# Kernel optimization log

Hardware: AMD Instinct MI355X
Metric: run time of the kernel (lower is better)

Reference implementation:

```python
import jax, jax.numpy as jnp
import numpy as np

N_NODES = 40000
N_EDGES = 640000
IN_C = 128
HID = 32
HEADS = 4
OUT_C = 8
NUM_GRAPHS = 64
NEG_SLOPE = 0.2


def setup_inputs() -> dict:
    key = jax.random.key(0)
    ks = jax.random.split(key, 16)
    x = jax.random.normal(ks[0], (N_NODES, IN_C), dtype=jnp.float32)
    edge_index = jax.random.randint(ks[1], (2, N_EDGES), 0, N_NODES, dtype=jnp.int64)
    batch = jnp.sort(jax.random.randint(ks[2], (N_NODES,), 0, NUM_GRAPHS, dtype=jnp.int64))
    s = lambda k, shape, fan_in: jax.random.normal(k, shape, jnp.float32) / np.sqrt(fan_in)
    # conv0: in -> hid, 4 heads, concat
    W0 = s(ks[3], (IN_C, HEADS * HID), IN_C)
    a_src0 = s(ks[4], (HEADS, HID), HID)
    a_dst0 = s(ks[5], (HEADS, HID), HID)
    b0 = jnp.zeros((HEADS * HID,), jnp.float32)
    # conv1: hid*H -> hid, 4 heads, concat
    W1 = s(ks[6], (HEADS * HID, HEADS * HID), HEADS * HID)
    a_src1 = s(ks[7], (HEADS, HID), HID)
    a_dst1 = s(ks[8], (HEADS, HID), HID)
    b1 = jnp.zeros((HEADS * HID,), jnp.float32)
    # conv2: hid*H -> hid, 1 head, no concat
    W2 = s(ks[9], (HEADS * HID, HID), HEADS * HID)
    a_src2 = s(ks[10], (1, HID), HID)
    a_dst2 = s(ks[11], (1, HID), HID)
    b2 = jnp.zeros((HID,), jnp.float32)
    lin1_w = s(ks[12], (HID, IN_C), HID)
    lin1_b = jnp.zeros((IN_C,), jnp.float32)
    lin2_w = s(ks[13], (IN_C, OUT_C), IN_C)
    lin2_b = jnp.zeros((OUT_C,), jnp.float32)
    return dict(x=x, edge_index=edge_index, batch=batch,
                W0=W0, a_src0=a_src0, a_dst0=a_dst0, b0=b0,
                W1=W1, a_src1=a_src1, a_dst1=a_dst1, b1=b1,
                W2=W2, a_src2=a_src2, a_dst2=a_dst2, b2=b2,
                lin1_w=lin1_w, lin1_b=lin1_b, lin2_w=lin2_w, lin2_b=lin2_b)


def gat_conv(x, src, dst, W, a_src, a_dst, b, heads, out_c, concat):
    N = x.shape[0]
    h = (x @ W).reshape(N, heads, out_c)          # [N,H,C]
    als = (h * a_src[None]).sum(-1)               # [N,H]
    ald = (h * a_dst[None]).sum(-1)               # [N,H]
    e = jax.nn.leaky_relu(als[src] + ald[dst], NEG_SLOPE)  # [E,H]
    m = jax.ops.segment_max(e, dst, num_segments=N)
    m = jnp.where(jnp.isfinite(m), m, 0.0)
    p = jnp.exp(e - m[dst])                       # [E,H]
    denom = jax.ops.segment_sum(p, dst, num_segments=N)
    alpha = p / jnp.maximum(denom[dst], 1e-16)
    out = jax.ops.segment_sum(h[src] * alpha[:, :, None], dst, num_segments=N)
    out = out.reshape(N, heads * out_c) if concat else out.mean(axis=1)
    return out + b


def reference(x, edge_index, batch,
              W0, a_src0, a_dst0, b0,
              W1, a_src1, a_dst1, b1,
              W2, a_src2, a_dst2, b2,
              lin1_w, lin1_b, lin2_w, lin2_b):
    N = x.shape[0]
    # PyG GATConv adds self-loops by default
    loop = jnp.arange(N, dtype=edge_index.dtype)
    src = jnp.concatenate([edge_index[0], loop])
    dst = jnp.concatenate([edge_index[1], loop])
    # eval mode: dropout is identity
    h = jax.nn.elu(gat_conv(x, src, dst, W0, a_src0, a_dst0, b0, HEADS, HID, True))
    h = jax.nn.elu(gat_conv(h, src, dst, W1, a_src1, a_dst1, b1, HEADS, HID, True))
    h = jax.nn.elu(gat_conv(h, src, dst, W2, a_src2, a_dst2, b2, 1, HID, False))
    # global mean pool over graphs
    sums = jax.ops.segment_sum(h, batch, num_segments=NUM_GRAPHS)
    cnts = jax.ops.segment_sum(jnp.ones((N, 1), h.dtype), batch, num_segments=NUM_GRAPHS)
    g = sums / jnp.maximum(cnts, 1.0)             # [G, HID]
    g = jax.nn.relu(g @ lin1_w + lin1_b)
    return g @ lin2_w + lin2_b                    # [G, OUT_C]
```

## Files before the change

kernel.cpp:

```cpp
#include <hip/hip_runtime.h>
#include <hip/hip_bf16.h>

#define N_NODES 40000
#define N_EDGES 640000
#define E_TOT   (N_EDGES + N_NODES)
#define NUM_GRAPHS 64
#define SCAN_BLOCKS 160
#define SCAN_CHUNK  250

#define CVTX_BLOCKS 5000
#define CVTW_BLOCKS 144
#define ZERO_INTS   (N_NODES + NUM_GRAPHS * 32 + NUM_GRAPHS)
#define ZERO_BLOCKS ((ZERO_INTS + 255) / 256)

typedef __attribute__((ext_vector_type(8))) short bf16x8;
typedef __attribute__((ext_vector_type(4))) float f32x4;

__device__ inline float bf2f(unsigned short u) {
    union { unsigned int i; float f; } v; v.i = ((unsigned int)u) << 16; return v.f;
}
__device__ inline unsigned short f2bf(float f) {
    union { float f; unsigned int i; } v; v.f = f;
    unsigned int r = v.i + 0x7FFF + ((v.i >> 16) & 1);
    return (unsigned short)(r >> 16);
}


__global__ __launch_bounds__(256) void setup_kernel(const float* __restrict__ x,
                                                    const float* __restrict__ W0,
                                                    const float* __restrict__ W1,
                                                    const float* __restrict__ W2,
                                                    unsigned short* __restrict__ Xb,
                                                    unsigned short* __restrict__ Wt0,
                                                    unsigned short* __restrict__ Wt1,
                                                    unsigned short* __restrict__ Wt2,
                                                    int* __restrict__ zbase) {
    int b = blockIdx.x;
    int tid = threadIdx.x;
    if (b < CVTX_BLOCKS) {
        int i = b * 256 + tid;
        float4 v = ((const float4*)x)[i];
        ushort4 o;
        o.x = f2bf(v.x); o.y = f2bf(v.y); o.z = f2bf(v.z); o.w = f2bf(v.w);
        ((ushort4*)Xb)[i] = o;
    } else if (b < CVTX_BLOCKS + CVTW_BLOCKS) {
        int idx = (b - CVTX_BLOCKS) * 256 + tid;
        if (idx < 16384) {
            int n = idx >> 7, k = idx & 127;
            Wt0[idx] = f2bf(W0[k * 128 + n]);
        } else if (idx < 32768) {
            int i = idx - 16384;
            int n = i >> 7, k = i & 127;
            Wt1[i] = f2bf(W1[k * 128 + n]);
        } else {
            int i = idx - 32768;
            int n = i >> 7, k = i & 127;
            Wt2[i] = f2bf(W2[k * 32 + n]);
        }
    } else {
        int i = (b - CVTX_BLOCKS - CVTW_BLOCKS) * 256 + tid;
        if (i < ZERO_INTS) zbase[i] = 0;
    }
}


__global__ __launch_bounds__(256) void hist_rank_kernel(const int* __restrict__ edst,
                                                        int* __restrict__ counts,
                                                        int* __restrict__ rank) {
    int e = blockIdx.x * 256 + threadIdx.x;
    if (e >= E_TOT) return;
    int d = (e < N_EDGES) ? edst[e] : (e - N_EDGES);
    rank[e] = atomicAdd(&counts[d], 1);
}

__global__ __launch_bounds__(256) void bsum_kernel(const int* __restrict__ counts,
                                                   int* __restrict__ bsum) {
    __shared__ int ws[4];
    int b = blockIdx.x, tid = threadIdx.x;
    int idx = b * SCAN_CHUNK + tid;
    int v = (tid < SCAN_CHUNK) ? counts[idx] : 0;
#pragma unroll
    for (int off = 32; off >= 1; off >>= 1) v += __shfl_down(v, off, 64);
    if ((tid & 63) == 0) ws[tid >> 6] = v;
    __syncthreads();
    if (tid == 0) bsum[b] = ws[0] + ws[1] + ws[2] + ws[3];
}

__global__ __launch_bounds__(256) void bscan_kernel(const int* __restrict__ bsum,
                                                    int* __restrict__ bofs) {
    __shared__ int s[256];
    int tid = threadIdx.x;
    int v = (tid < SCAN_BLOCKS) ? bsum[tid] : 0;
    s[tid] = v;
    __syncthreads();
    for (int off = 1; off < 256; off <<= 1) {
        int t = (tid >= off) ? s[tid - off] : 0;
        __syncthreads();
        s[tid] += t;
        __syncthreads();
    }
    if (tid < SCAN_BLOCKS) bofs[tid] = s[tid] - v;
}

__global__ __launch_bounds__(256) void boffs_kernel(const int* __restrict__ counts,
                                                    const int* __restrict__ bofs,
                                                    int* __restrict__ offs) {
    __shared__ int s[256];
    int b = blockIdx.x, tid = threadIdx.x;
    int idx = b * SCAN_CHUNK + tid;
    int v = (tid < SCAN_CHUNK) ? counts[idx] : 0;
    s[tid] = v;
    __syncthreads();
    for (int off = 1; off < 256; off <<= 1) {
        int t = (tid >= off) ? s[tid - off] : 0;
        __syncthreads();
        s[tid] += t;
        __syncthreads();
    }
    int incl = s[tid];
    int base = bofs[b];
    if (tid < SCAN_CHUNK) {
        offs[idx] = base + incl - v;
        if (idx == N_NODES - 1) offs[N_NODES] = base + incl;
    }
}

__global__ __launch_bounds__(256) void scatter_kernel(const int* __restrict__ esrc,
                                                      const int* __restrict__ edst,
                                                      const int* __restrict__ offs,
                                                      const int* __restrict__ rank,
                                                      int* __restrict__ ssrc) {
    int e = blockIdx.x * 256 + threadIdx.x;
    if (e >= E_TOT) return;
    int d, s;
    if (e < N_EDGES) { d = edst[e]; s = esrc[e]; }
    else             { d = e - N_EDGES; s = d; }
    ssrc[offs[d] + rank[e]] = s;
}

__global__ __launch_bounds__(256) void gemm128_mfma(const unsigned short* __restrict__ Xb,
                                                    const unsigned short* __restrict__ Wt,
                                                    const float* __restrict__ asrc,
                                                    const float* __restrict__ adst,
                                                    unsigned short* __restrict__ Hb,
                                                    float* __restrict__ ALS_t,
                                                    float* __restrict__ ALD_t) {
    int wave = threadIdx.x >> 6;
    int lane = threadIdx.x & 63;
    int l15 = lane & 15;
    int q = lane >> 4;
    int r0 = (blockIdx.x * 4 + wave) * 16;

    f32x4 acc[8];
#pragma unroll
    for (int t = 0; t < 8; ++t) acc[t] = (f32x4){0.f, 0.f, 0.f, 0.f};

    float asv[8], adv[8];
#pragma unroll
    for (int t = 0; t < 8; ++t) {
        int c = t * 16 + l15;
        asv[t] = asrc[c];
        adv[t] = adst[c];
    }

    const unsigned short* xrow = Xb + (long)(r0 + l15) * 128 + q * 8;
    const unsigned short* wrow = Wt + (long)l15 * 128 + q * 8;
#pragma unroll
    for (int kt = 0; kt < 4; ++kt) {
        bf16x8 a = *(const bf16x8*)(xrow + kt * 32);
#pragma unroll
        for (int t = 0; t < 8; ++t) {
            bf16x8 b = *(const bf16x8*)(wrow + (long)t * 16 * 128 + kt * 32);
            acc[t] = __builtin_amdgcn_mfma_f32_16x16x32_bf16(a, b, acc[t], 0, 0, 0);
        }
    }

#pragma unroll
    for (int t = 0; t < 8; ++t)
#pragma unroll
        for (int i = 0; i < 4; ++i)
            Hb[(long)(r0 + q * 4 + i) * 128 + t * 16 + l15] = f2bf(acc[t][i]);

#pragma unroll
    for (int i = 0; i < 4; ++i) {
        float ps0 = acc[0][i] * asv[0] + acc[1][i] * asv[1];
        float ps1 = acc[2][i] * asv[2] + acc[3][i] * asv[3];
        float ps2 = acc[4][i] * asv[4] + acc[5][i] * asv[5];
        float ps3 = acc[6][i] * asv[6] + acc[7][i] * asv[7];
        float pd0 = acc[0][i] * adv[0] + acc[1][i] * adv[1];
        float pd1 = acc[2][i] * adv[2] + acc[3][i] * adv[3];
        float pd2 = acc[4][i] * adv[4] + acc[5][i] * adv[5];
        float pd3 = acc[6][i] * adv[6] + acc[7][i] * adv[7];
#pragma unroll
        for (int m = 1; m < 16; m <<= 1) {
            ps0 += __shfl_xor(ps0, m, 16); ps1 += __shfl_xor(ps1, m, 16);
            ps2 += __shfl_xor(ps2, m, 16); ps3 += __shfl_xor(ps3, m, 16);
            pd0 += __shfl_xor(pd0, m, 16); pd1 += __shfl_xor(pd1, m, 16);
            pd2 += __shfl_xor(pd2, m, 16); pd3 += __shfl_xor(pd3, m, 16);
        }
        int r = r0 + q * 4 + i;
        if (l15 < 4) {
            float v = (l15 == 0) ? ps0 : (l15 == 1) ? ps1 : (l15 == 2) ? ps2 : ps3;
            ALS_t[l15 * N_NODES + r] = v;
        } else if (l15 < 8) {
            int h = l15 - 4;
            float v = (h == 0) ? pd0 : (h == 1) ? pd1 : (h == 2) ? pd2 : pd3;
            ALD_t[h * N_NODES + r] = v;
        }
    }
}

__global__ __launch_bounds__(256) void gemm32_mfma(const unsigned short* __restrict__ Xb,
                                                   const unsigned short* __restrict__ Wt2,
                                                   const float* __restrict__ asrc,
                                                   const float* __restrict__ adst,
                                                   unsigned short* __restrict__ H2b,
                                                   float* __restrict__ ALS,
                                                   float* __restrict__ ALD) {
    int wave = threadIdx.x >> 6;
    int lane = threadIdx.x & 63;
    int l15 = lane & 15;
    int q = lane >> 4;
    int r0 = (blockIdx.x * 4 + wave) * 16;

    f32x4 acc[2];
    acc[0] = (f32x4){0.f, 0.f, 0.f, 0.f};
    acc[1] = (f32x4){0.f, 0.f, 0.f, 0.f};

    const unsigned short* xrow = Xb + (long)(r0 + l15) * 128 + q * 8;
    const unsigned short* wrow = Wt2 + (long)l15 * 128 + q * 8;
#pragma unroll
    for (int kt = 0; kt < 4; ++kt) {
        bf16x8 a = *(const bf16x8*)(xrow + kt * 32);
#pragma unroll
        for (int t = 0; t < 2; ++t) {
            bf16x8 b = *(const bf16x8*)(wrow + (long)t * 16 * 128 + kt * 32);
            acc[t] = __builtin_amdgcn_mfma_f32_16x16x32_bf16(a, b, acc[t], 0, 0, 0);
        }
    }

    float as0 = asrc[l15], as1 = asrc[16 + l15];
    float ad0 = adst[l15], ad1 = adst[16 + l15];
#pragma unroll
    for (int t = 0; t < 2; ++t)
#pragma unroll
        for (int i = 0; i < 4; ++i)
            H2b[(long)(r0 + q * 4 + i) * 32 + t * 16 + l15] = f2bf(acc[t][i]);

#pragma unroll
    for (int i = 0; i < 4; ++i) {
        float ps = acc[0][i] * as0 + acc[1][i] * as1;
        float pd = acc[0][i] * ad0 + acc[1][i] * ad1;
#pragma unroll
        for (int m = 1; m < 16; m <<= 1) {
            ps += __shfl_xor(ps, m, 16);
            pd += __shfl_xor(pd, m, 16);
        }
        if (l15 == 0) {
            int r = r0 + q * 4 + i;
            ALS[r] = ps;
            ALD[r] = pd;
        }
    }
}

__global__ __launch_bounds__(256) void agg128(const unsigned short* __restrict__ Hb,
                                              const float* __restrict__ ALS_t,
                                              const float* __restrict__ ALD_t,
                                              const int* __restrict__ offs,
                                              const int* __restrict__ ssrc,
                                              const float* __restrict__ bias,
                                              unsigned short* __restrict__ OUTb) {
    int n = blockIdx.x * 4 + (threadIdx.x >> 6);
    n = __builtin_amdgcn_readfirstlane(n);
    if (n >= N_NODES) return;
    int lane = threadIdx.x & 63;
    int c = lane * 2;
    int head = lane >> 4;
    int e16 = lane & 15;
    float aldh = ALD_t[head * N_NODES + n];
    const float* alsh = ALS_t + (long)head * N_NODES;
    int j0 = __builtin_amdgcn_readfirstlane(offs[n]);
    int j1 = __builtin_amdgcn_readfirstlane(offs[n + 1]);
    float a0 = 0.f, a1 = 0.f, dsum = 0.f;
    for (int jb = j0; jb < j1; jb += 16) {
        int j = jb + e16;
        int jc = (j < j1) ? j : (j1 - 1);
        int s = ssrc[jc];
        float e = alsh[s] + aldh;
        e = (e > 0.f) ? e : 0.2f * e;
        float w = (j < j1) ? __expf(e) : 0.f;
        int st[16]; float wt[16];
#pragma unroll
        for (int t = 0; t < 16; ++t) {
            st[t] = __shfl(s, t, 16);
            wt[t] = __shfl(w, t, 16);
        }
        unsigned int hv[16];
#pragma unroll
        for (int t = 0; t < 16; ++t)
            hv[t] = *(const unsigned int*)(Hb + (long)st[t] * 128 + c);
#pragma unroll
        for (int t = 0; t < 16; ++t) {
            float h0 = bf2f((unsigned short)(hv[t] & 0xFFFF));
            float h1 = bf2f((unsigned short)(hv[t] >> 16));
            dsum += wt[t];
            a0 += wt[t] * h0;
            a1 += wt[t] * h1;
        }
    }
    float inv = 1.0f / dsum;
    float o0 = a0 * inv + bias[c];
    float o1 = a1 * inv + bias[c + 1];
    o0 = (o0 > 0.f) ? o0 : (__expf(o0) - 1.f);
    o1 = (o1 > 0.f) ? o1 : (__expf(o1) - 1.f);
    ushort2 ob; ob.x = f2bf(o0); ob.y = f2bf(o1);
    *(ushort2*)(OUTb + (long)n * 128 + c) = ob;
}

__global__ __launch_bounds__(256) void agg32(const unsigned short* __restrict__ H2b,
                                             const float* __restrict__ ALS,
                                             const float* __restrict__ ALD,
                                             const int* __restrict__ offs,
                                             const int* __restrict__ ssrc,
                                             const float* __restrict__ bias,
                                             float* __restrict__ OUT) {
    int wv = blockIdx.x * 4 + (threadIdx.x >> 6);
    int lane = threadIdx.x & 63;
    int col = lane & 31;
    int half = lane >> 5;
    int e16 = lane & 15;
    int n = wv * 2 + half;
    if (n >= N_NODES) return;
    float aldn = ALD[n];
    int j0 = offs[n], j1 = offs[n + 1];
    float a = 0.f, dsum = 0.f;
    for (int jb = j0; jb < j1; jb += 16) {
        int j = jb + e16;
        int jc = (j < j1) ? j : (j1 - 1);
        int s = ssrc[jc];
        float e = ALS[s] + aldn;
        e = (e > 0.f) ? e : 0.2f * e;
        float w = (j < j1) ? __expf(e) : 0.f;
        int st[16]; float wt[16];
#pragma unroll
        for (int t = 0; t < 16; ++t) {
            st[t] = __shfl(s, t, 16);
            wt[t] = __shfl(w, t, 16);
        }
        unsigned short hv[16];
#pragma unroll
        for (int t = 0; t < 16; ++t)
            hv[t] = H2b[st[t] * 32 + col];
#pragma unroll
        for (int t = 0; t < 16; ++t) {
            dsum += wt[t];
            a += wt[t] * bf2f(hv[t]);
        }
    }
    float o = a / dsum + bias[col];
    o = (o > 0.f) ? o : (__expf(o) - 1.f);
    OUT[n * 32 + col] = o;
}

__global__ __launch_bounds__(256) void pool_kernel(const float* __restrict__ H3,
                                                   const int* __restrict__ batch,
                                                   float* __restrict__ gsum,
                                                   float* __restrict__ gcnt) {
    const int CHUNK = 40;
    int gid = (blockIdx.x * 256 + threadIdx.x) >> 5;
    int c = threadIdx.x & 31;
    int n0 = gid * CHUNK;
    if (n0 >= N_NODES) return;
    int n1 = n0 + CHUNK;
    if (n1 > N_NODES) n1 = N_NODES;
    int cur = batch[n0];
    float acc = 0.f;
    int cnt = 0;
    for (int n = n0; n < n1; ++n) {
        int b = batch[n];
        if (b != cur) {
            atomicAdd(&gsum[cur * 32 + c], acc);
            if (c == 0) atomicAdd(&gcnt[cur], (float)cnt);
            cur = b; acc = 0.f; cnt = 0;
        }
        acc += H3[n * 32 + c];
        cnt++;
    }
    atomicAdd(&gsum[cur * 32 + c], acc);
    if (c == 0) atomicAdd(&gcnt[cur], (float)cnt);
}

__global__ __launch_bounds__(256) void mlp_kernel(const float* __restrict__ gsum,
                                                  const float* __restrict__ gcnt,
                                                  const float* __restrict__ l1w,
                                                  const float* __restrict__ l1b,
                                                  const float* __restrict__ l2w,
                                                  const float* __restrict__ l2b,
                                                  float* __restrict__ out) {
    __shared__ float g[NUM_GRAPHS * 32];
    __shared__ float t1[NUM_GRAPHS * 128];
    int tid = threadIdx.x;
    for (int i = tid; i < NUM_GRAPHS * 32; i += 256) {
        float c = gcnt[i >> 5];
        g[i] = gsum[i] / fmaxf(c, 1.0f);
    }
    __syncthreads();
    for (int i = tid; i < NUM_GRAPHS * 128; i += 256) {
        int r = i >> 7, j = i & 127;
        float a = l1b[j];
        for (int k = 0; k < 32; ++k) a += g[r * 32 + k] * l1w[k * 128 + j];
        t1[i] = fmaxf(a, 0.f);
    }
    __syncthreads();
    for (int i = tid; i < NUM_GRAPHS * 8; i += 256) {
        int r = i >> 3, j = i & 7;
        float a = l2b[j];
        for (int k = 0; k < 128; ++k) a += t1[r * 128 + k] * l2w[k * 8 + j];
        out[i] = a;
    }
}


extern "C" void kernel_launch(void* const* d_in, const int* in_sizes, int n_in,
                              void* d_out, int out_size, void* d_ws, size_t ws_size,
                              hipStream_t stream) {
    const float* x      = (const float*)d_in[0];
    const int*   eidx   = (const int*)d_in[1];
    const int*   batch  = (const int*)d_in[2];
    const float* W0     = (const float*)d_in[3];
    const float* asrc0  = (const float*)d_in[4];
    const float* adst0  = (const float*)d_in[5];
    const float* b0     = (const float*)d_in[6];
    const float* W1     = (const float*)d_in[7];
    const float* asrc1  = (const float*)d_in[8];
    const float* adst1  = (const float*)d_in[9];
    const float* b1     = (const float*)d_in[10];
    const float* W2     = (const float*)d_in[11];
    const float* asrc2  = (const float*)d_in[12];
    const float* adst2  = (const float*)d_in[13];
    const float* b2     = (const float*)d_in[14];
    const float* l1w    = (const float*)d_in[15];
    const float* l1b    = (const float*)d_in[16];
    const float* l2w    = (const float*)d_in[17];
    const float* l2b    = (const float*)d_in[18];
    float* out = (float*)d_out;

    const int* esrc = eidx;
    const int* edst = eidx + N_EDGES;

    float* ALS  = (float*)d_ws;
    float* ALD  = ALS + N_NODES * 4;
    float* h3   = ALD + N_NODES * 4;
    int* counts = (int*)(h3 + (long)N_NODES * 32);
    float* gsum = (float*)(counts + N_NODES);
    float* gcnt = gsum + NUM_GRAPHS * 32;
    int* offs   = (int*)(gcnt + NUM_GRAPHS);
    int* bsum   = offs + (N_NODES + 1);
    int* bofs   = bsum + SCAN_BLOCKS;
    int* rank   = bofs + SCAN_BLOCKS;
    int* ssrc   = rank + E_TOT;
    uintptr_t p = (uintptr_t)(ssrc + E_TOT);
    p = (p + 15) & ~(uintptr_t)15;
    unsigned short* Xb   = (unsigned short*)p;
    unsigned short* Hb   = Xb + (long)N_NODES * 128;
    unsigned short* OUTb = Hb + (long)N_NODES * 128;
    unsigned short* H2b  = OUTb + (long)N_NODES * 128;
    unsigned short* Wt0  = H2b + (long)N_NODES * 32;
    unsigned short* Wt1  = Wt0 + 128 * 128;
    unsigned short* Wt2  = Wt1 + 128 * 128;

    setup_kernel<<<CVTX_BLOCKS + CVTW_BLOCKS + ZERO_BLOCKS, 256, 0, stream>>>(
        x, W0, W1, W2, Xb, Wt0, Wt1, Wt2, counts);

    int eblocks = (E_TOT + 255) / 256;
    hist_rank_kernel<<<eblocks, 256, 0, stream>>>(edst, counts, rank);
    bsum_kernel<<<SCAN_BLOCKS, 256, 0, stream>>>(counts, bsum);
    bscan_kernel<<<1, 256, 0, stream>>>(bsum, bofs);
    boffs_kernel<<<SCAN_BLOCKS, 256, 0, stream>>>(counts, bofs, offs);
    scatter_kernel<<<eblocks, 256, 0, stream>>>(esrc, edst, offs, rank, ssrc);

    gemm128_mfma<<<625, 256, 0, stream>>>(Xb, Wt0, asrc0, adst0, Hb, ALS, ALD);
    agg128<<<10000, 256, 0, stream>>>(Hb, ALS, ALD, offs, ssrc, b0, OUTb);

    gemm128_mfma<<<625, 256, 0, stream>>>(OUTb, Wt1, asrc1, adst1, Hb, ALS, ALD);
    agg128<<<10000, 256, 0, stream>>>(Hb, ALS, ALD, offs, ssrc, b1, OUTb);

    gemm32_mfma<<<625, 256, 0, stream>>>(OUTb, Wt2, asrc2, adst2, H2b, ALS, ALD);
    agg32<<<5000, 256, 0, stream>>>(H2b, ALS, ALD, offs, ssrc, b2, h3);

    pool_kernel<<<125, 256, 0, stream>>>(h3, batch, gsum, gcnt);
    mlp_kernel<<<1, 256, 0, stream>>>(gsum, gcnt, l1w, l1b, l2w, l2b, out);
}
```

Baseline: 313.5 us.

## Split hidden features into per-head planes and aggregate one head per wave

The GEMM now writes its output as four head-major planes of 32 bf16 columns per node instead of one 128-wide row. The 128-wide aggregation launches four times as many blocks, one per (head, block of nodes). Each wave handles one head, with its four 16-lane groups gathering different neighbours, and the partial sums are reduced across groups with shuffles. The intent is smaller per-head working sets for better cache locality and more parallelism for the gather. The cost is redundant index and offset loads per head, extra shuffles, and only 16 of 64 lanes doing the final store.

```diff
diff --git a/kernel.cpp b/kernel.cpp
--- a/kernel.cpp
+++ b/kernel.cpp
@@ -142,7 +142,7 @@
                                                     const unsigned short* __restrict__ Wt,
                                                     const float* __restrict__ asrc,
                                                     const float* __restrict__ adst,
-                                                    unsigned short* __restrict__ Hb,
+                                                    unsigned short* __restrict__ Hq,
                                                     float* __restrict__ ALS_t,
                                                     float* __restrict__ ALD_t) {
     int wave = threadIdx.x >> 6;
@@ -176,10 +176,12 @@
     }
 
 #pragma unroll
-    for (int t = 0; t < 8; ++t)
+    for (int t = 0; t < 8; ++t) {
+        unsigned short* hq = Hq + (long)(t >> 1) * N_NODES * 32;
 #pragma unroll
         for (int i = 0; i < 4; ++i)
-            Hb[(long)(r0 + q * 4 + i) * 128 + t * 16 + l15] = f2bf(acc[t][i]);
+            hq[(long)(r0 + q * 4 + i) * 32 + (t & 1) * 16 + l15] = f2bf(acc[t][i]);
+    }
 
 #pragma unroll
     for (int i = 0; i < 4; ++i) {
@@ -264,22 +266,22 @@
     }
 }
 
-__global__ __launch_bounds__(256) void agg128(const unsigned short* __restrict__ Hb,
+__global__ __launch_bounds__(256) void agg128(const unsigned short* __restrict__ Hq,
                                               const float* __restrict__ ALS_t,
                                               const float* __restrict__ ALD_t,
                                               const int* __restrict__ offs,
                                               const int* __restrict__ ssrc,
                                               const float* __restrict__ bias,
                                               unsigned short* __restrict__ OUTb) {
-    int n = blockIdx.x * 4 + (threadIdx.x >> 6);
+    int p = blockIdx.x / 10000;
+    int n = (blockIdx.x % 10000) * 4 + (threadIdx.x >> 6);
     n = __builtin_amdgcn_readfirstlane(n);
-    if (n >= N_NODES) return;
     int lane = threadIdx.x & 63;
-    int c = lane * 2;
-    int head = lane >> 4;
     int e16 = lane & 15;
-    float aldh = ALD_t[head * N_NODES + n];
-    const float* alsh = ALS_t + (long)head * N_NODES;
+    int g = lane >> 4;
+    const unsigned short* hbase = Hq + (long)p * N_NODES * 32;
+    const float* alsh = ALS_t + (long)p * N_NODES;
+    float aldh = ALD_t[p * N_NODES + n];
     int j0 = __builtin_amdgcn_readfirstlane(offs[n]);
     int j1 = __builtin_amdgcn_readfirstlane(offs[n + 1]);
     float a0 = 0.f, a1 = 0.f, dsum = 0.f;
@@ -287,35 +289,37 @@
         int j = jb + e16;
         int jc = (j < j1) ? j : (j1 - 1);
         int s = ssrc[jc];
+        unsigned int hv[4];
+#pragma unroll
+        for (int r = 0; r < 4; ++r) {
+            int se = __shfl(s, 4 * r + g, 16);
+            hv[r] = *(const unsigned int*)(hbase + (long)se * 32 + e16 * 2);
+        }
         float e = alsh[s] + aldh;
         e = (e > 0.f) ? e : 0.2f * e;
         float w = (j < j1) ? __expf(e) : 0.f;
-        int st[16]; float wt[16];
-#pragma unroll
-        for (int t = 0; t < 16; ++t) {
-            st[t] = __shfl(s, t, 16);
-            wt[t] = __shfl(w, t, 16);
-        }
-        unsigned int hv[16];
-#pragma unroll
-        for (int t = 0; t < 16; ++t)
-            hv[t] = *(const unsigned int*)(Hb + (long)st[t] * 128 + c);
-#pragma unroll
-        for (int t = 0; t < 16; ++t) {
-            float h0 = bf2f((unsigned short)(hv[t] & 0xFFFF));
-            float h1 = bf2f((unsigned short)(hv[t] >> 16));
-            dsum += wt[t];
-            a0 += wt[t] * h0;
-            a1 += wt[t] * h1;
-        }
-    }
+        dsum += w;
+#pragma unroll
+        for (int r = 0; r < 4; ++r) {
+            float we = __shfl(w, 4 * r + g, 16);
+            a0 += we * bf2f((unsigned short)(hv[r] & 0xFFFF));
+            a1 += we * bf2f((unsigned short)(hv[r] >> 16));
+        }
+    }
+    a0 += __shfl_xor(a0, 16); a0 += __shfl_xor(a0, 32);
+    a1 += __shfl_xor(a1, 16); a1 += __shfl_xor(a1, 32);
+#pragma unroll
+    for (int m = 1; m < 16; m <<= 1) dsum += __shfl_xor(dsum, m, 16);
     float inv = 1.0f / dsum;
+    int c = p * 32 + e16 * 2;
     float o0 = a0 * inv + bias[c];
     float o1 = a1 * inv + bias[c + 1];
     o0 = (o0 > 0.f) ? o0 : (__expf(o0) - 1.f);
     o1 = (o1 > 0.f) ? o1 : (__expf(o1) - 1.f);
-    ushort2 ob; ob.x = f2bf(o0); ob.y = f2bf(o1);
-    *(ushort2*)(OUTb + (long)n * 128 + c) = ob;
+    if (lane < 16) {
+        ushort2 ob; ob.x = f2bf(o0); ob.y = f2bf(o1);
+        *(ushort2*)(OUTb + (long)n * 128 + c) = ob;
+    }
 }
 
 __global__ __launch_bounds__(256) void agg32(const unsigned short* __restrict__ H2b,
@@ -463,8 +467,8 @@
     uintptr_t p = (uintptr_t)(ssrc + E_TOT);
     p = (p + 15) & ~(uintptr_t)15;
     unsigned short* Xb   = (unsigned short*)p;
-    unsigned short* Hb   = Xb + (long)N_NODES * 128;
-    unsigned short* OUTb = Hb + (long)N_NODES * 128;
+    unsigned short* Hq   = Xb + (long)N_NODES * 128;
+    unsigned short* OUTb = Hq + (long)N_NODES * 128;
     unsigned short* H2b  = OUTb + (long)N_NODES * 128;
     unsigned short* Wt0  = H2b + (long)N_NODES * 32;
     unsigned short* Wt1  = Wt0 + 128 * 128;
@@ -480,11 +484,11 @@
     boffs_kernel<<<SCAN_BLOCKS, 256, 0, stream>>>(counts, bofs, offs);
     scatter_kernel<<<eblocks, 256, 0, stream>>>(esrc, edst, offs, rank, ssrc);
 
-    gemm128_mfma<<<625, 256, 0, stream>>>(Xb, Wt0, asrc0, adst0, Hb, ALS, ALD);
-    agg128<<<10000, 256, 0, stream>>>(Hb, ALS, ALD, offs, ssrc, b0, OUTb);
-
-    gemm128_mfma<<<625, 256, 0, stream>>>(OUTb, Wt1, asrc1, adst1, Hb, ALS, ALD);
-    agg128<<<10000, 256, 0, stream>>>(Hb, ALS, ALD, offs, ssrc, b1, OUTb);
+    gemm128_mfma<<<625, 256, 0, stream>>>(Xb, Wt0, asrc0, adst0, Hq, ALS, ALD);
+    agg128<<<40000, 256, 0, stream>>>(Hq, ALS, ALD, offs, ssrc, b0, OUTb);
+
+    gemm128_mfma<<<625, 256, 0, stream>>>(OUTb, Wt1, asrc1, adst1, Hq, ALS, ALD);
+    agg128<<<40000, 256, 0, stream>>>(Hq, ALS, ALD, offs, ssrc, b1, OUTb);
 
     gemm32_mfma<<<625, 256, 0, stream>>>(OUTb, Wt2, asrc2, adst2, H2b, ALS, ALD);
     agg32<<<5000, 256, 0, stream>>>(H2b, ALS, ALD, offs, ssrc, b2, h3);
```

Result: slower. 360.7 us (+15.1%).

## Merge histogram into setup kernel and scatter into first GEMM launch

Applied to the files above, without the earlier changes.

Zeroing of the counts buffer moves to hipMemsetAsync, which lets the edge histogram/rank atomics run as extra blocks of the setup conversion kernel. The CSR scatter pass is likewise appended as extra blocks of the first-layer GEMM kernel, since the two are independent. This removes two kernel launches and lets independent work overlap within one grid. In exchange it adds a memset call and block-index branching, and it mixes heterogeneous block types in one grid.

```diff
diff --git a/kernel.cpp b/kernel.cpp
--- a/kernel.cpp
+++ b/kernel.cpp
@@ -10,8 +10,9 @@
 
 #define CVTX_BLOCKS 5000
 #define CVTW_BLOCKS 144
-#define ZERO_INTS   (N_NODES + NUM_GRAPHS * 32 + NUM_GRAPHS)
-#define ZERO_BLOCKS ((ZERO_INTS + 255) / 256)
+#define SETUP_BLOCKS (CVTX_BLOCKS + CVTW_BLOCKS)
+#define EBLOCKS ((E_TOT + 255) / 256)
+#define GEMM_BLOCKS 625
 
 typedef __attribute__((ext_vector_type(8))) short bf16x8;
 typedef __attribute__((ext_vector_type(4))) float f32x4;
@@ -26,15 +27,17 @@
 }
 
 
-__global__ __launch_bounds__(256) void setup_kernel(const float* __restrict__ x,
-                                                    const float* __restrict__ W0,
-                                                    const float* __restrict__ W1,
-                                                    const float* __restrict__ W2,
-                                                    unsigned short* __restrict__ Xb,
-                                                    unsigned short* __restrict__ Wt0,
-                                                    unsigned short* __restrict__ Wt1,
-                                                    unsigned short* __restrict__ Wt2,
-                                                    int* __restrict__ zbase) {
+__global__ __launch_bounds__(256) void setup_hist_kernel(const float* __restrict__ x,
+                                                         const float* __restrict__ W0,
+                                                         const float* __restrict__ W1,
+                                                         const float* __restrict__ W2,
+                                                         unsigned short* __restrict__ Xb,
+                                                         unsigned short* __restrict__ Wt0,
+                                                         unsigned short* __restrict__ Wt1,
+                                                         unsigned short* __restrict__ Wt2,
+                                                         const int* __restrict__ edst,
+                                                         int* __restrict__ counts,
+                                                         int* __restrict__ rank) {
     int b = blockIdx.x;
     int tid = threadIdx.x;
     if (b < CVTX_BLOCKS) {
@@ -43,7 +46,7 @@
         ushort4 o;
         o.x = f2bf(v.x); o.y = f2bf(v.y); o.z = f2bf(v.z); o.w = f2bf(v.w);
         ((ushort4*)Xb)[i] = o;
-    } else if (b < CVTX_BLOCKS + CVTW_BLOCKS) {
+    } else if (b < SETUP_BLOCKS) {
         int idx = (b - CVTX_BLOCKS) * 256 + tid;
         if (idx < 16384) {
             int n = idx >> 7, k = idx & 127;
@@ -52,26 +55,20 @@
             int i = idx - 16384;
             int n = i >> 7, k = i & 127;
             Wt1[i] = f2bf(W1[k * 128 + n]);
-        } else {
+        } else if (idx < 36864) {
             int i = idx - 32768;
             int n = i >> 7, k = i & 127;
             Wt2[i] = f2bf(W2[k * 32 + n]);
         }
     } else {
-        int i = (b - CVTX_BLOCKS - CVTW_BLOCKS) * 256 + tid;
-        if (i < ZERO_INTS) zbase[i] = 0;
-    }
-}
-
-
-__global__ __launch_bounds__(256) void hist_rank_kernel(const int* __restrict__ edst,
-                                                        int* __restrict__ counts,
-                                                        int* __restrict__ rank) {
-    int e = blockIdx.x * 256 + threadIdx.x;
-    if (e >= E_TOT) return;
-    int d = (e < N_EDGES) ? edst[e] : (e - N_EDGES);
-    rank[e] = atomicAdd(&counts[d], 1);
-}
+        int e = (b - SETUP_BLOCKS) * 256 + tid;
+        if (e < E_TOT) {
+            int d = (e < N_EDGES) ? edst[e] : (e - N_EDGES);
+            rank[e] = atomicAdd(&counts[d], 1);
+        }
+    }
+}
+
 
 __global__ __launch_bounds__(256) void bsum_kernel(const int* __restrict__ counts,
                                                    int* __restrict__ bsum) {
@@ -125,31 +122,20 @@
     }
 }
 
-__global__ __launch_bounds__(256) void scatter_kernel(const int* __restrict__ esrc,
-                                                      const int* __restrict__ edst,
-                                                      const int* __restrict__ offs,
-                                                      const int* __restrict__ rank,
-                                                      int* __restrict__ ssrc) {
-    int e = blockIdx.x * 256 + threadIdx.x;
-    if (e >= E_TOT) return;
-    int d, s;
-    if (e < N_EDGES) { d = edst[e]; s = esrc[e]; }
-    else             { d = e - N_EDGES; s = d; }
-    ssrc[offs[d] + rank[e]] = s;
-}
-
-__global__ __launch_bounds__(256) void gemm128_mfma(const unsigned short* __restrict__ Xb,
-                                                    const unsigned short* __restrict__ Wt,
-                                                    const float* __restrict__ asrc,
-                                                    const float* __restrict__ adst,
-                                                    unsigned short* __restrict__ Hb,
-                                                    float* __restrict__ ALS_t,
-                                                    float* __restrict__ ALD_t) {
+
+__device__ __forceinline__ void gemm128_body(int blk,
+                                             const unsigned short* __restrict__ Xb,
+                                             const unsigned short* __restrict__ Wt,
+                                             const float* __restrict__ asrc,
+                                             const float* __restrict__ adst,
+                                             unsigned short* __restrict__ Hb,
+                                             float* __restrict__ ALS_t,
+                                             float* __restrict__ ALD_t) {
     int wave = threadIdx.x >> 6;
     int lane = threadIdx.x & 63;
     int l15 = lane & 15;
     int q = lane >> 4;
-    int r0 = (blockIdx.x * 4 + wave) * 16;
+    int r0 = (blk * 4 + wave) * 16;
 
     f32x4 acc[8];
 #pragma unroll
@@ -208,6 +194,42 @@
             ALD_t[h * N_NODES + r] = v;
         }
     }
+}
+
+__global__ __launch_bounds__(256) void gemm_scatter_kernel(const unsigned short* __restrict__ Xb,
+                                                           const unsigned short* __restrict__ Wt,
+                                                           const float* __restrict__ asrc,
+                                                           const float* __restrict__ adst,
+                                                           unsigned short* __restrict__ Hb,
+                                                           float* __restrict__ ALS_t,
+                                                           float* __restrict__ ALD_t,
+                                                           const int* __restrict__ esrc,
+                                                           const int* __restrict__ edst,
+                                                           const int* __restrict__ offs,
+                                                           const int* __restrict__ rank,
+                                                           int* __restrict__ ssrc) {
+    int b = blockIdx.x;
+    if (b < GEMM_BLOCKS) {
+        gemm128_body(b, Xb, Wt, asrc, adst, Hb, ALS_t, ALD_t);
+    } else {
+        int e = (b - GEMM_BLOCKS) * 256 + threadIdx.x;
+        if (e < E_TOT) {
+            int d, s;
+            if (e < N_EDGES) { d = edst[e]; s = esrc[e]; }
+            else             { d = e - N_EDGES; s = d; }
+            ssrc[offs[d] + rank[e]] = s;
+        }
+    }
+}
+
+__global__ __launch_bounds__(256) void gemm128_mfma(const unsigned short* __restrict__ Xb,
+                                                    const unsigned short* __restrict__ Wt,
+                                                    const float* __restrict__ asrc,
+                                                    const float* __restrict__ adst,
+                                                    unsigned short* __restrict__ Hb,
+                                                    float* __restrict__ ALS_t,
+                                                    float* __restrict__ ALD_t) {
+    gemm128_body(blockIdx.x, Xb, Wt, asrc, adst, Hb, ALS_t, ALD_t);
 }
 
 __global__ __launch_bounds__(256) void gemm32_mfma(const unsigned short* __restrict__ Xb,
@@ -470,23 +492,23 @@
     unsigned short* Wt1  = Wt0 + 128 * 128;
     unsigned short* Wt2  = Wt1 + 128 * 128;
 
-    setup_kernel<<<CVTX_BLOCKS + CVTW_BLOCKS + ZERO_BLOCKS, 256, 0, stream>>>(
-        x, W0, W1, W2, Xb, Wt0, Wt1, Wt2, counts);
-
-    int eblocks = (E_TOT + 255) / 256;
-    hist_rank_kernel<<<eblocks, 256, 0, stream>>>(edst, counts, rank);
+    size_t zbytes = (size_t)(N_NODES + NUM_GRAPHS * 32 + NUM_GRAPHS) * 4;
+    hipMemsetAsync(counts, 0, zbytes, stream);
+    setup_hist_kernel<<<SETUP_BLOCKS + EBLOCKS, 256, 0, stream>>>(
+        x, W0, W1, W2, Xb, Wt0, Wt1, Wt2, edst, counts, rank);
+
     bsum_kernel<<<SCAN_BLOCKS, 256, 0, stream>>>(counts, bsum);
     bscan_kernel<<<1, 256, 0, stream>>>(bsum, bofs);
     boffs_kernel<<<SCAN_BLOCKS, 256, 0, stream>>>(counts, bofs, offs);
-    scatter_kernel<<<eblocks, 256, 0, stream>>>(esrc, edst, offs, rank, ssrc);
-
-    gemm128_mfma<<<625, 256, 0, stream>>>(Xb, Wt0, asrc0, adst0, Hb, ALS, ALD);
+
+    gemm_scatter_kernel<<<GEMM_BLOCKS + EBLOCKS, 256, 0, stream>>>(
+        Xb, Wt0, asrc0, adst0, Hb, ALS, ALD, esrc, edst, offs, rank, ssrc);
     agg128<<<10000, 256, 0, stream>>>(Hb, ALS, ALD, offs, ssrc, b0, OUTb);
 
-    gemm128_mfma<<<625, 256, 0, stream>>>(OUTb, Wt1, asrc1, adst1, Hb, ALS, ALD);
+    gemm128_mfma<<<GEMM_BLOCKS, 256, 0, stream>>>(OUTb, Wt1, asrc1, adst1, Hb, ALS, ALD);
     agg128<<<10000, 256, 0, stream>>>(Hb, ALS, ALD, offs, ssrc, b1, OUTb);
 
-    gemm32_mfma<<<625, 256, 0, stream>>>(OUTb, Wt2, asrc2, adst2, H2b, ALS, ALD);
+    gemm32_mfma<<<GEMM_BLOCKS, 256, 0, stream>>>(OUTb, Wt2, asrc2, adst2, H2b, ALS, ALD);
     agg32<<<5000, 256, 0, stream>>>(H2b, ALS, ALD, offs, ssrc, b2, h3);
 
     pool_kernel<<<125, 256, 0, stream>>>(h3, batch, gsum, gcnt);
```

Result: faster. 307.0 us (-2.1%).
